# Kernel optimization log

Measured on AMD Instinct MI355X. Metric: run time of the kernel, lower is better.

## Reference

```python
import jax, jax.numpy as jnp
import numpy as np

_SAMPLING_EPS = 1e-5


def setup_inputs() -> dict:
    key = jax.random.key(0)
    ks = jax.random.split(key, 7)
    N, V, H = 256, 128000, 200  # num_seqs, vocab_size, output-history length
    logits = jax.random.normal(ks[0], (N, V), dtype=jnp.float32)
    output_tokens = jax.random.randint(ks[1], (N, H), 0, V, dtype=jnp.int32)
    presence_penalties = jax.random.uniform(ks[2], (N,), jnp.float32, 0.0, 2.0)
    frequency_penalties = jax.random.uniform(ks[3], (N,), jnp.float32, 0.0, 2.0)
    temperatures = jax.random.uniform(ks[4], (N,), jnp.float32, 0.5, 1.5)
    top_ps = jax.random.uniform(ks[5], (N,), jnp.float32, 0.5, 1.0)
    top_ks = jax.random.randint(ks[6], (N,), 1, 1000, dtype=jnp.int32)
    return {
        "logits": logits,
        "presence_penalties": presence_penalties,
        "frequency_penalties": frequency_penalties,
        "temperatures": temperatures,
        "top_ps": top_ps,
        "output_tokens": output_tokens,
        "top_ks": top_ks,
    }


def reference(logits, presence_penalties, frequency_penalties, temperatures,
              top_ps, output_tokens, top_ks):
    N, V = logits.shape

    # ---- _apply_penalties: bincount of previously generated tokens per row ----
    rows = jnp.arange(N)[:, None]  # [N,1] broadcast against [N,H] token ids
    bin_counts = jnp.zeros((N, V), logits.dtype).at[rows, output_tokens].add(1.0)
    # rows are skipped when both penalties are < eps (original builds an index list)
    active = ((presence_penalties >= _SAMPLING_EPS) |
              (frequency_penalties >= _SAMPLING_EPS))[:, None]
    presence_mask = (bin_counts > 0.0).astype(logits.dtype)
    penalty = (frequency_penalties[:, None] * bin_counts
               + presence_penalties[:, None] * presence_mask)
    logits = logits - jnp.where(active, penalty, jnp.zeros((), logits.dtype))

    # ---- temperature scaling + softmax ----
    logits = logits / temperatures[:, None]
    probs = jax.nn.softmax(logits, axis=-1)

    # ---- _apply_top_p_top_k: sort desc, cumsum, mask, unsort ----
    probs_idx = jnp.argsort(-probs, axis=-1)                    # descending order
    probs_sort = jnp.take_along_axis(probs, probs_idx, axis=-1)
    probs_sum = jnp.cumsum(probs_sort, axis=-1)
    top_p_mask = (probs_sum - probs_sort) > top_ps[:, None]     # exclusive cumsum > p
    probs_sort = jnp.where(top_p_mask, 0.0, probs_sort)
    top_k_mask = jnp.arange(V, dtype=top_ks.dtype)[None, :] >= top_ks[:, None]
    probs_sort = jnp.where(top_k_mask, 0.0, probs_sort)
    inv_idx = jnp.argsort(probs_idx, axis=-1)                   # unsort permutation
    filtered_probs = jnp.take_along_axis(probs_sort, inv_idx, axis=-1)
    return filtered_probs
```

## Files before the change

kernel.cpp:

```cpp
#include <hip/hip_runtime.h>
#include <stdint.h>

#define NB 8192
#define BSHIFT 19
#define HS 512
#define HM 511
#define CAP 4096
#define PCAP 2048
#define NRB 2048
#define NT 1024

typedef unsigned long long ull;

__device__ __forceinline__ unsigned mono_u32(float x) {
    unsigned b = __float_as_uint(x);
    return (b & 0x80000000u) ? ~b : (b | 0x80000000u);
}
__device__ __forceinline__ float inv_mono(unsigned u) {
    unsigned b = (u & 0x80000000u) ? (u & 0x7fffffffu) : ~u;
    return __uint_as_float(b);
}

__device__ __forceinline__ float compute_x(float l, int cnt,
                                           float pres, float freq, float t) {
    float pen = __fadd_rn(__fmul_rn(freq, (float)cnt), (cnt > 0) ? pres : 0.0f);
    return __fdiv_rn(__fsub_rn(l, pen), t);
}

__global__ __launch_bounds__(NT) void k_fused(
    const float* __restrict__ logits, const int* __restrict__ tokens,
    const float* __restrict__ pres_v, const float* __restrict__ freq_v,
    const float* __restrict__ temps, const float* __restrict__ topp_v,
    const int* __restrict__ topk_v, int V, int H, float* __restrict__ out)
{
    __shared__ __align__(16) char smem[(32 + 16 + 8 + 4) * 1024];
    unsigned* hc = (unsigned*)smem;
    ull* skey = (ull*)smem;
    char* regB = smem + 32 * 1024;
    float* se = (float*)regB;
    ull* tmpc = (ull*)regB;
    char* regC = smem + 48 * 1024;
    unsigned* rh = (unsigned*)regC;
    char* regD = smem + 56 * 1024;
    int* hkey = (int*)regD;
    int* hval = (int*)(regD + 2 * 1024);
    __shared__ int wt_i[16];
    __shared__ float wt_f[16];
    __shared__ float esum_s, corr_s;
    __shared__ int bstar_s, lcnt_s, rb_s, pcnt_s;

    int row = blockIdx.x, tid = threadIdx.x;
    int lane = tid & 63, wid = tid >> 6;
    for (int b = tid; b < NB; b += NT) hc[b] = 0u;
    if (tid == 0) { esum_s = 0.f; corr_s = 0.f; bstar_s = -1; lcnt_s = 0; rb_s = 0; pcnt_s = 0; }

    for (int i = tid; i < HS; i += NT) { hkey[i] = -1; hval[i] = 0; }
    __syncthreads();
    const int* trow = tokens + (size_t)row * H;
    for (int i = tid; i < H; i += NT) {
        int v = trow[i];
        unsigned h = ((unsigned)v * 2654435761u) >> 23;
        while (true) {
            int prev = atomicCAS(&hkey[h], -1, v);
            if (prev == -1 || prev == v) { atomicAdd(&hval[h], 1); break; }
            h = (h + 1) & HM;
        }
    }
    __syncthreads();

    float t = temps[row];
    float r = __fdiv_rn(1.0f, t);
    const float* lrow = logits + (size_t)row * V;
    const float4* l4p = (const float4*)lrow;
    float4* o4p = (float4*)(out + (size_t)row * V);
    const float4 z4 = make_float4(0.f, 0.f, 0.f, 0.f);
    int V4 = V >> 2;

    float es = 0.0f;
    int i = tid;
    for (; i + 7 * NT < V4; i += 8 * NT) {
        float4 arr[8];
#pragma unroll
        for (int q = 0; q < 8; ++q) arr[q] = l4p[i + q * NT];
#pragma unroll
        for (int q = 0; q < 8; ++q) o4p[i + q * NT] = z4;
#pragma unroll
        for (int q = 0; q < 8; ++q)
#pragma unroll
            for (int j = 0; j < 4; ++j) {
                float x = __fmul_rn((&arr[q].x)[j], r);
                atomicAdd(&hc[mono_u32(x) >> BSHIFT], 1u);
                es += __expf(x);
            }
    }
    for (; i < V4; i += NT) {
        float4 A = l4p[i];
        o4p[i] = z4;
#pragma unroll
        for (int j = 0; j < 4; ++j) {
            float x = __fmul_rn((&A.x)[j], r);
            atomicAdd(&hc[mono_u32(x) >> BSHIFT], 1u);
            es += __expf(x);
        }
    }
    for (int v = (V4 << 2) + tid; v < V; v += NT) {
        float x = __fmul_rn(lrow[v], r);
        out[(size_t)row * V + v] = 0.0f;
        atomicAdd(&hc[mono_u32(x) >> BSHIFT], 1u);
        es += __expf(x);
    }
    for (int off = 32; off; off >>= 1) es += __shfl_down(es, off);
    if ((tid & 63) == 0) atomicAdd(&esum_s, es);
    __syncthreads();

    float pres = pres_v[row], freq = freq_v[row];
    int active = (pres >= 1e-5f) || (freq >= 1e-5f);
    float corr = 0.0f;
    if (active) {
        for (int s = tid; s < HS; s += NT) {
            int v = hkey[s];
            if (v >= 0) {
                int c = hval[s];
                float l = lrow[v];
                float x0 = __fmul_rn(l, r);
                float xp = compute_x(l, c, pres, freq, t);
                unsigned b0 = mono_u32(x0) >> BSHIFT;
                unsigned bp = mono_u32(xp) >> BSHIFT;
                if (b0 != bp) { atomicSub(&hc[b0], 1u); atomicAdd(&hc[bp], 1u); }
                corr += __expf(xp) - __expf(x0);
            }
        }
    }
    for (int off = 32; off; off >>= 1) corr += __shfl_down(corr, off);
    if ((tid & 63) == 0) atomicAdd(&corr_s, corr);
    __syncthreads();

    const int BPT = NB / NT;
    int base = tid * BPT;
    int acc = 0;
#pragma unroll
    for (int q = BPT - 1; q >= 0; --q) { acc += (int)hc[base + q]; hc[base + q] = (unsigned)acc; }
    int k = topk_v[row];
    {
        int v = acc;
#pragma unroll
        for (int off = 1; off < 64; off <<= 1) {
            int o = __shfl_down(v, off);
            if (lane + off < 64) v += o;
        }
        if (lane == 0) wt_i[wid] = v;
        __syncthreads();
        int above = v - acc;
#pragma unroll
        for (int w = 0; w < 16; ++w) if (w > wid) above += wt_i[w];
        int best = -1;
#pragma unroll
        for (int q = BPT - 1; q >= 0; --q)
            if ((int)hc[base + q] + above >= k) { best = base + q; break; }
        if (best >= 0) atomicMax(&bstar_s, best);
    }
    __syncthreads();
    int bst = bstar_s - 2;
    if (bst < 0) bst = 0;
    float Sp = esum_s + corr_s;
    __syncthreads();

    i = tid;
    for (; i + 7 * NT < V4; i += 8 * NT) {
        float4 arr[8];
#pragma unroll
        for (int q = 0; q < 8; ++q) arr[q] = l4p[i + q * NT];
#pragma unroll
        for (int q = 0; q < 8; ++q) {
            int vb = (i + q * NT) << 2;
#pragma unroll
            for (int j = 0; j < 4; ++j) {
                float l = (&arr[q].x)[j];
                unsigned ua = mono_u32(__fmul_rn(l, r));
                if ((int)(ua >> BSHIFT) >= bst) {
                    unsigned ue = mono_u32(__fdiv_rn(l, t));
                    int pos = atomicAdd(&lcnt_s, 1);
                    if (pos < CAP)
                        skey[pos] = ((ull)ue << 32) | (unsigned)~(unsigned)(vb + j);
                }
            }
        }
    }
    for (; i < V4; i += NT) {
        float4 A = l4p[i];
#pragma unroll
        for (int j = 0; j < 4; ++j) {
            float l = (&A.x)[j];
            unsigned ua = mono_u32(__fmul_rn(l, r));
            if ((int)(ua >> BSHIFT) >= bst) {
                unsigned ue = mono_u32(__fdiv_rn(l, t));
                int pos = atomicAdd(&lcnt_s, 1);
                if (pos < CAP)
                    skey[pos] = ((ull)ue << 32) | (unsigned)~(unsigned)((i << 2) + j);
            }
        }
    }
    for (int v = (V4 << 2) + tid; v < V; v += NT) {
        float l = lrow[v];
        unsigned ua = mono_u32(__fmul_rn(l, r));
        if ((int)(ua >> BSHIFT) >= bst) {
            unsigned ue = mono_u32(__fdiv_rn(l, t));
            int pos = atomicAdd(&lcnt_s, 1);
            if (pos < CAP)
                skey[pos] = ((ull)ue << 32) | (unsigned)~(unsigned)v;
        }
    }
    __syncthreads();
    int count = lcnt_s; if (count > CAP) count = CAP;

    if (active) {
        for (int j = tid; j < count; j += NT) {
            unsigned idx = ~(unsigned)(skey[j] & 0xffffffffull);
            unsigned h = (idx * 2654435761u) >> 23;
            int c = 0;
            while (true) {
                int kk = hkey[h];
                if (kk == (int)idx) { c = hval[h]; break; }
                if (kk == -1) break;
                h = (h + 1) & HM;
            }
            if (c > 0) {
                float xp = compute_x(lrow[idx], c, pres, freq, t);
                skey[j] = ((ull)mono_u32(xp) << 32) | (unsigned)~idx;
            }
        }
    }
    __syncthreads();
    for (int g = tid; g < NRB; g += NT) rh[g] = 0u;
    __syncthreads();
    int gmin = bst << 6;
    for (int j = tid; j < count; j += NT) {
        unsigned u = (unsigned)(skey[j] >> 32);
        int rel = (int)(u >> 13) - gmin;
        rel = rel < 0 ? 0 : (rel > NRB - 1 ? NRB - 1 : rel);
        atomicAdd(&rh[rel], 1u);
    }
    __syncthreads();
    {
        int b2i = tid * 2;
        int a2 = (int)rh[b2i + 1];
        rh[b2i + 1] = (unsigned)a2;
        a2 += (int)rh[b2i];
        rh[b2i] = (unsigned)a2;
        int v = a2;
#pragma unroll
        for (int off = 1; off < 64; off <<= 1) {
            int o = __shfl_down(v, off);
            if (lane + off < 64) v += o;
        }
        if (lane == 0) wt_i[wid] = v;
        __syncthreads();
        int above = v - a2;
#pragma unroll
        for (int w = 0; w < 16; ++w) if (w > wid) above += wt_i[w];
        int best = -1;
        if ((int)rh[b2i + 1] + above >= k) best = b2i + 1;
        else if ((int)rh[b2i] + above >= k) best = b2i;
        if (best >= 0) atomicMax(&rb_s, best);
    }
    __syncthreads();
    int rb = rb_s;
    for (int j = tid; j < count; j += NT) {
        unsigned u = (unsigned)(skey[j] >> 32);
        int rel = (int)(u >> 13) - gmin;
        rel = rel < 0 ? 0 : (rel > NRB - 1 ? NRB - 1 : rel);
        if (rel >= rb) {
            int pos = atomicAdd(&pcnt_s, 1);
            if (pos < PCAP) tmpc[pos] = skey[j];
        }
    }
    __syncthreads();
    int count2 = pcnt_s;
    if (count2 <= PCAP) {
        for (int j = tid; j < count2; j += NT) skey[j] = tmpc[j];
        count = count2;
    }
    __syncthreads();

    int m = 1; while (m < count) m <<= 1;
    for (int j = count + tid; j < m; j += NT) skey[j] = 0ull;
    __syncthreads();
    for (int kk = 2; kk <= m; kk <<= 1) {
        for (int jj = kk >> 1; jj > 0; jj >>= 1) {
            for (int i2 = tid; i2 < m; i2 += NT) {
                int ixj = i2 ^ jj;
                if (ixj > i2) {
                    ull A = skey[i2], B = skey[ixj];
                    bool up = ((i2 & kk) != 0);
                    if ((A > B) == up) { skey[i2] = B; skey[ixj] = A; }
                }
            }
            __syncthreads();
        }
    }

    for (int j = tid; j < CAP; j += NT)
        se[j] = (j < count) ? __expf(inv_mono((unsigned)(skey[j] >> 32))) : 0.0f;
    __syncthreads();
    int j0 = tid << 2;
    float e0 = se[j0], e1 = se[j0 + 1], e2 = se[j0 + 2], e3 = se[j0 + 3];
    float c0 = e0, c1 = c0 + e1, c2 = c1 + e2, c3 = c2 + e3;
    float vf = c3;
#pragma unroll
    for (int off = 1; off < 64; off <<= 1) {
        float o = __shfl_up(vf, off);
        if (lane >= off) vf += o;
    }
    if (lane == 63) wt_f[wid] = vf;
    __syncthreads();
    float pre = vf - c3;
#pragma unroll
    for (int w = 0; w < 16; ++w) if (w < wid) pre += wt_f[w];

    float pS = topp_v[row] * Sp;
    float inc[4] = {pre + c0, pre + c1, pre + c2, pre + c3};
    float ee[4] = {e0, e1, e2, e3};
#pragma unroll
    for (int q = 0; q < 4; ++q) {
        int j = j0 + q;
        if (j < count) {
            float e = ee[q];
            float excl = __fsub_rn(inc[q], e);
            if ((j < k) && (excl <= pS)) {
                unsigned idx = ~(unsigned)(skey[j] & 0xffffffffull);
                out[(size_t)row * V + idx] = __fdiv_rn(e, Sp);
            }
        }
    }
}

extern "C" void kernel_launch(void* const* d_in, const int* in_sizes, int n_in,
                              void* d_out, int out_size, void* d_ws, size_t ws_size,
                              hipStream_t stream) {
    const float* logits = (const float*)d_in[0];
    const float* pres   = (const float*)d_in[1];
    const float* freq   = (const float*)d_in[2];
    const float* temps  = (const float*)d_in[3];
    const float* topps  = (const float*)d_in[4];
    const int*   tokens = (const int*)d_in[5];
    const int*   topks  = (const int*)d_in[6];
    int N = in_sizes[1];
    int V = in_sizes[0] / N;
    int H = in_sizes[5] / N;
    float* out = (float*)d_out;

    k_fused<<<N, NT, 0, stream>>>(logits, tokens, pres, freq, temps, topps,
                                  topks, V, H, out);
}
```

Before: 308.8 us.

## Capture high-logit candidates in first pass and overlap output zeroing with sort

During the first pass over each row, indices of logits at or above a fixed threshold are appended to a shared-memory candidate buffer. When that buffer did not overflow and the threshold bucket lies below the top-k boundary bucket, the second full scan of the row is replaced by a scan of only these candidates. Zeroing of the output row is moved out of the first pass and spread across the bitonic sort stages, so the stores can overlap with sort work. The cost is an extra contended shared atomic per candidate in the first pass, and a buffer that extends past its original region into space used later; the full scan remains as a fallback when the conditions fail.

Measured after the change: 282.2 us. -8.6%, faster.

```diff
diff --git a/kernel.cpp b/kernel.cpp
--- a/kernel.cpp
+++ b/kernel.cpp
@@ -6,9 +6,11 @@
 #define HS 512
 #define HM 511
 #define CAP 4096
+#define CAP2 6144
 #define PCAP 2048
 #define NRB 2048
 #define NT 1024
+#define CAPTHR 1.75f
 
 typedef unsigned long long ull;
 
@@ -41,18 +43,22 @@
     ull* tmpc = (ull*)regB;
     char* regC = smem + 48 * 1024;
     unsigned* rh = (unsigned*)regC;
+    unsigned* cbuf = (unsigned*)regB;
     char* regD = smem + 56 * 1024;
     int* hkey = (int*)regD;
     int* hval = (int*)(regD + 2 * 1024);
     __shared__ int wt_i[16];
     __shared__ float wt_f[16];
     __shared__ float esum_s, corr_s;
-    __shared__ int bstar_s, lcnt_s, rb_s, pcnt_s;
+    __shared__ int bstar_s, lcnt_s, rb_s, pcnt_s, cap_s;
 
     int row = blockIdx.x, tid = threadIdx.x;
     int lane = tid & 63, wid = tid >> 6;
     for (int b = tid; b < NB; b += NT) hc[b] = 0u;
-    if (tid == 0) { esum_s = 0.f; corr_s = 0.f; bstar_s = -1; lcnt_s = 0; rb_s = 0; pcnt_s = 0; }
+    if (tid == 0) {
+        esum_s = 0.f; corr_s = 0.f; bstar_s = -1;
+        lcnt_s = 0; rb_s = 0; pcnt_s = 0; cap_s = 0;
+    }
 
     for (int i = tid; i < HS; i += NT) { hkey[i] = -1; hval[i] = 0; }
     __syncthreads();
@@ -75,6 +81,8 @@
     float4* o4p = (float4*)(out + (size_t)row * V);
     const float4 z4 = make_float4(0.f, 0.f, 0.f, 0.f);
     int V4 = V >> 2;
+    int ZITER = (V4 + NT - 1) / NT;
+    int zc = 0;
 
     float es = 0.0f;
     int i = tid;
@@ -83,31 +91,44 @@
 #pragma unroll
         for (int q = 0; q < 8; ++q) arr[q] = l4p[i + q * NT];
 #pragma unroll
-        for (int q = 0; q < 8; ++q) o4p[i + q * NT] = z4;
-#pragma unroll
-        for (int q = 0; q < 8; ++q)
+        for (int q = 0; q < 8; ++q) {
+            int vb = (i + q * NT) << 2;
 #pragma unroll
             for (int j = 0; j < 4; ++j) {
-                float x = __fmul_rn((&arr[q].x)[j], r);
+                float l = (&arr[q].x)[j];
+                float x = __fmul_rn(l, r);
                 atomicAdd(&hc[mono_u32(x) >> BSHIFT], 1u);
                 es += __expf(x);
-            }
+                if (l >= CAPTHR) {
+                    int pos = atomicAdd(&cap_s, 1);
+                    if (pos < CAP2) cbuf[pos] = (unsigned)(vb + j);
+                }
+            }
+        }
     }
     for (; i < V4; i += NT) {
         float4 A = l4p[i];
-        o4p[i] = z4;
 #pragma unroll
         for (int j = 0; j < 4; ++j) {
-            float x = __fmul_rn((&A.x)[j], r);
+            float l = (&A.x)[j];
+            float x = __fmul_rn(l, r);
             atomicAdd(&hc[mono_u32(x) >> BSHIFT], 1u);
             es += __expf(x);
+            if (l >= CAPTHR) {
+                int pos = atomicAdd(&cap_s, 1);
+                if (pos < CAP2) cbuf[pos] = (unsigned)((i << 2) + j);
+            }
         }
     }
     for (int v = (V4 << 2) + tid; v < V; v += NT) {
-        float x = __fmul_rn(lrow[v], r);
-        out[(size_t)row * V + v] = 0.0f;
+        float l = lrow[v];
+        float x = __fmul_rn(l, r);
         atomicAdd(&hc[mono_u32(x) >> BSHIFT], 1u);
         es += __expf(x);
+        if (l >= CAPTHR) {
+            int pos = atomicAdd(&cap_s, 1);
+            if (pos < CAP2) cbuf[pos] = (unsigned)v;
+        }
     }
     for (int off = 32; off; off >>= 1) es += __shfl_down(es, off);
     if ((tid & 63) == 0) atomicAdd(&esum_s, es);
@@ -163,51 +184,81 @@
     int bst = bstar_s - 2;
     if (bst < 0) bst = 0;
     float Sp = esum_s + corr_s;
-    __syncthreads();
-
-    i = tid;
-    for (; i + 7 * NT < V4; i += 8 * NT) {
-        float4 arr[8];
-#pragma unroll
-        for (int q = 0; q < 8; ++q) arr[q] = l4p[i + q * NT];
-#pragma unroll
-        for (int q = 0; q < 8; ++q) {
-            int vb = (i + q * NT) << 2;
-#pragma unroll
-            for (int j = 0; j < 4; ++j) {
-                float l = (&arr[q].x)[j];
+    int ccount = cap_s;
+    __syncthreads();
+
+    int lb = (int)(mono_u32(__fmul_rn(CAPTHR, r)) >> BSHIFT);
+    bool skip_c = (ccount <= CAP2) && (lb < bst);
+
+    if (skip_c) {
+        unsigned myidx[6];
+#pragma unroll
+        for (int q = 0; q < 6; ++q) {
+            int j2 = tid + q * NT;
+            myidx[q] = (j2 < ccount) ? cbuf[j2] : 0xffffffffu;
+        }
+        float myl[6];
+#pragma unroll
+        for (int q = 0; q < 6; ++q)
+            if (myidx[q] != 0xffffffffu) myl[q] = lrow[myidx[q]];
+#pragma unroll
+        for (int q = 0; q < 6; ++q) {
+            if (myidx[q] != 0xffffffffu) {
+                float l = myl[q];
                 unsigned ua = mono_u32(__fmul_rn(l, r));
                 if ((int)(ua >> BSHIFT) >= bst) {
                     unsigned ue = mono_u32(__fdiv_rn(l, t));
                     int pos = atomicAdd(&lcnt_s, 1);
                     if (pos < CAP)
-                        skey[pos] = ((ull)ue << 32) | (unsigned)~(unsigned)(vb + j);
+                        skey[pos] = ((ull)ue << 32) | (unsigned)~myidx[q];
                 }
             }
         }
-    }
-    for (; i < V4; i += NT) {
-        float4 A = l4p[i];
-#pragma unroll
-        for (int j = 0; j < 4; ++j) {
-            float l = (&A.x)[j];
+    } else {
+        i = tid;
+        for (; i + 7 * NT < V4; i += 8 * NT) {
+            float4 arr[8];
+#pragma unroll
+            for (int q = 0; q < 8; ++q) arr[q] = l4p[i + q * NT];
+#pragma unroll
+            for (int q = 0; q < 8; ++q) {
+                int vb = (i + q * NT) << 2;
+#pragma unroll
+                for (int j = 0; j < 4; ++j) {
+                    float l = (&arr[q].x)[j];
+                    unsigned ua = mono_u32(__fmul_rn(l, r));
+                    if ((int)(ua >> BSHIFT) >= bst) {
+                        unsigned ue = mono_u32(__fdiv_rn(l, t));
+                        int pos = atomicAdd(&lcnt_s, 1);
+                        if (pos < CAP)
+                            skey[pos] = ((ull)ue << 32) | (unsigned)~(unsigned)(vb + j);
+                    }
+                }
+            }
+        }
+        for (; i < V4; i += NT) {
+            float4 A = l4p[i];
+#pragma unroll
+            for (int j = 0; j < 4; ++j) {
+                float l = (&A.x)[j];
+                unsigned ua = mono_u32(__fmul_rn(l, r));
+                if ((int)(ua >> BSHIFT) >= bst) {
+                    unsigned ue = mono_u32(__fdiv_rn(l, t));
+                    int pos = atomicAdd(&lcnt_s, 1);
+                    if (pos < CAP)
+                        skey[pos] = ((ull)ue << 32) | (unsigned)~(unsigned)((i << 2) + j);
+                }
+            }
+        }
+        for (int v = (V4 << 2) + tid; v < V; v += NT) {
+            float l = lrow[v];
             unsigned ua = mono_u32(__fmul_rn(l, r));
             if ((int)(ua >> BSHIFT) >= bst) {
                 unsigned ue = mono_u32(__fdiv_rn(l, t));
                 int pos = atomicAdd(&lcnt_s, 1);
                 if (pos < CAP)
-                    skey[pos] = ((ull)ue << 32) | (unsigned)~(unsigned)((i << 2) + j);
-            }
-        }
-    }
-    for (int v = (V4 << 2) + tid; v < V; v += NT) {
-        float l = lrow[v];
-        unsigned ua = mono_u32(__fmul_rn(l, r));
-        if ((int)(ua >> BSHIFT) >= bst) {
-            unsigned ue = mono_u32(__fdiv_rn(l, t));
-            int pos = atomicAdd(&lcnt_s, 1);
-            if (pos < CAP)
-                skey[pos] = ((ull)ue << 32) | (unsigned)~(unsigned)v;
+                    skey[pos] = ((ull)ue << 32) | (unsigned)~(unsigned)v;
+            }
         }
     }
     __syncthreads();
@@ -287,6 +338,11 @@
     __syncthreads();
     for (int kk = 2; kk <= m; kk <<= 1) {
         for (int jj = kk >> 1; jj > 0; jj >>= 1) {
+            if (zc < ZITER) {
+                int p = tid + zc * NT;
+                if (p < V4) o4p[p] = z4;
+                ++zc;
+            }
             for (int i2 = tid; i2 < m; i2 += NT) {
                 int ixj = i2 ^ jj;
                 if (ixj > i2) {
@@ -298,6 +354,12 @@
             __syncthreads();
         }
     }
+    for (; zc < ZITER; ++zc) {
+        int p = tid + zc * NT;
+        if (p < V4) o4p[p] = z4;
+    }
+    for (int v2 = (V4 << 2) + tid; v2 < V; v2 += NT)
+        out[(size_t)row * V + v2] = 0.0f;
 
     for (int j = tid; j < CAP; j += NT)
         se[j] = (j < count) ? __expf(inv_mono((unsigned)(skey[j] >> 32))) : 0.0f;
```
